# Kernel optimization log

Measured on AMD Instinct MI355X. Metric: run time of the kernel, lower is better.

The kernel has to match this reference:

```python
import jax, jax.numpy as jnp
import numpy as np

IMG = 448; P = 16; C = 3; D = 512; DC = 8; DS = 4
NH = IMG // P            # 28 patches per side
NPATCH = NH * NH         # 784
PDIM = C * P * P         # 768
BATCH = 32
EPS = 1e-5


def setup_inputs() -> dict:
    key = jax.random.key(0)
    ks = jax.random.split(key, 10)
    def lin(k, fan_in, shape):
        bound = 1.0 / np.sqrt(fan_in)
        return jax.random.uniform(k, shape, jnp.float32, -bound, bound)
    return {
        "images": jax.random.normal(ks[0], (BATCH, C, IMG, IMG), jnp.float32),
        "W_patch": lin(ks[1], PDIM, (PDIM, D)),
        "b_patch": jnp.zeros((D,), jnp.float32),
        "pos_embed": jax.random.normal(ks[2], (1, NPATCH, D), jnp.float32) * 0.02,
        "W_coord": lin(ks[3], D, (D, DC)),
        "b_coord": jnp.zeros((DC,), jnp.float32),
        "W_spinor": lin(ks[4], D, (D, DS)),
        "b_spinor": jnp.zeros((DS,), jnp.float32),
        "W_embed": lin(ks[5], DC, (DC, D)),
        "b_embed": jnp.zeros((D,), jnp.float32),
        "ln_gamma": jnp.ones((D,), jnp.float32),
        "ln_beta": jnp.zeros((D,), jnp.float32),
        "W_out": lin(ks[6], D, (D, D)),
        "b_out": jnp.zeros((D,), jnp.float32),
    }


def reference(images, W_patch, b_patch, pos_embed, W_coord, b_coord,
              W_spinor, b_spinor, W_embed, b_embed,
              ln_gamma, ln_beta, W_out, b_out):
    B = images.shape[0]
    # patchify == F.unfold(kernel=stride=P).transpose(1,2):
    # patches[b, bh*NH+bw, c*P*P + i*P + j] = images[b, c, bh*P+i, bw*P+j]
    patches = images.reshape(B, C, NH, P, NH, P)
    patches = patches.transpose(0, 2, 4, 1, 3, 5).reshape(B, NPATCH, PDIM)
    # patch embed + positional embedding  -> (B, NPATCH, D)
    x = patches @ W_patch + b_patch + pos_embed
    # manifold projection: coords (B,N,DC), spinor (B,N,DS)
    coords = x @ W_coord + b_coord
    spinor = x @ W_spinor + b_spinor
    # K0 scalar bilinear: psi^T psi -> (B, N)
    K0 = jnp.sum(spinor * spinor, axis=-1)
    # embed back from manifold coords -> (B, N, D)
    x_manifold = coords @ W_embed + b_embed
    # K0-modulated remix + residual
    x_enh = x_manifold * K0[..., None] + x
    # output projection: LayerNorm -> Linear
    mu = jnp.mean(x_enh, axis=-1, keepdims=True)
    var = jnp.mean(jnp.square(x_enh - mu), axis=-1, keepdims=True)
    x_norm = (x_enh - mu) * jax.lax.rsqrt(var + EPS) * ln_gamma + ln_beta
    return x_norm @ W_out + b_out
```

## Files before the change

kernel.cpp:

```cpp
#include <hip/hip_runtime.h>
#include <hip/hip_bf16.h>
#include <stdint.h>


typedef __bf16 bf16_t;
typedef bf16_t bf16x8 __attribute__((ext_vector_type(8)));
typedef bf16_t bf16x4 __attribute__((ext_vector_type(4)));
typedef float  f32x4  __attribute__((ext_vector_type(4)));

#define IMG     448
#define PSZ     16
#define NHP     28
#define NPATCH  784
#define PDIM    768
#define DMODEL  512
#define MROWS   25088

__device__ __forceinline__ void gload16(void* lds, const void* g) {
  __builtin_amdgcn_global_load_lds(
      (__attribute__((address_space(1))) void*)(uintptr_t)g,
      (__attribute__((address_space(3))) void*)lds,
      16, 0, 0);
}

__global__ __launch_bounds__(256) void transpose_to_bf16(
    const float* __restrict__ src, bf16_t* __restrict__ dst, int K, int N)
{
  __shared__ float t[64][65];
  const int tx = threadIdx.x;
  const int ty = threadIdx.y;
  const int bx = blockIdx.x * 64;
  const int by = blockIdx.y * 64;
  #pragma unroll
  for (int r = ty; r < 64; r += 4)
    t[r][tx] = src[(size_t)(by + r) * N + (bx + tx)];
  __syncthreads();
  #pragma unroll
  for (int r = ty; r < 64; r += 4)
    dst[(size_t)(bx + r) * K + (by + tx)] = (bf16_t)t[tx][r];
}

__global__ __launch_bounds__(256) void manifold_prep(
    const float* __restrict__ Wc, const float* __restrict__ Ws,
    bf16_t* __restrict__ Wcsg)
{
  const int idx = blockIdx.x * 256 + threadIdx.x;
  if (idx < 8192) {
    const int r = idx >> 9, n = idx & 511;
    float v = 0.f;
    if (r < 8)       v = Wc[n * 8 + r];
    else if (r < 12) v = Ws[n * 4 + (r - 8)];
    Wcsg[idx] = (bf16_t)v;
  }
}

__global__ __launch_bounds__(256) void patchify_bf16(
    const float* __restrict__ images, bf16_t* __restrict__ Apat)
{
  __shared__ bf16_t t[16][456];
  const int tid = threadIdx.x;
  const int bid = blockIdx.x;
  const int b = bid / 84, rem = bid % 84;
  const int c = rem / 28, ph = rem % 28;
  const float* src = images + ((size_t)(b * 3 + c) * IMG + ph * PSZ) * IMG;

  #pragma unroll
  for (int idx = tid; idx < 16 * 112; idx += 256) {
    const int i = idx / 112, x4 = idx % 112;
    const float4 v = *(const float4*)(src + (size_t)i * IMG + x4 * 4);
    bf16x4 w;
    w[0] = (bf16_t)v.x; w[1] = (bf16_t)v.y; w[2] = (bf16_t)v.z; w[3] = (bf16_t)v.w;
    *(bf16x4*)&t[i][x4 * 4] = w;
  }
  __syncthreads();

  const size_t mbase = (size_t)b * NPATCH + (size_t)ph * NHP;
  #pragma unroll
  for (int idx = tid; idx < 28 * 64; idx += 256) {
    const int pw = idx >> 6, e = idx & 63;
    const int i = e >> 2, j4 = e & 3;
    const bf16x4 w = *(const bf16x4*)&t[i][pw * 16 + j4 * 4];
    *(bf16x4*)&Apat[(mbase + pw) * PDIM + c * 256 + i * 16 + j4 * 4] = w;
  }
}

template<int KDIM, int EPI>
__global__ __launch_bounds__(256) void gemm_bf16(
    const bf16_t* __restrict__ A, const bf16_t* __restrict__ BT,
    const float* __restrict__ bias, const float* __restrict__ pos,
    void* __restrict__ outp)
{
  __shared__ bf16_t As[3 * 64 * 64];
  __shared__ bf16_t Bs[3 * 128 * 64];
  constexpr int ABUF = 64 * 64;
  constexpr int BBUF = 128 * 64;
  constexpr int NT = KDIM / 64;

  const int tid  = threadIdx.x;
  const int orig = blockIdx.x;
  const int wg   = (orig & 7) * 196 + (orig >> 3);
  const int n0   = (wg & 3) * 128;
  const int m0   = (wg >> 2) * 64;

  const int wave = tid >> 6, lane = tid & 63;

  const int ra = lane >> 3;
  const int ca = (lane & 7) ^ ra;
  const bf16_t* ag = A  + (size_t)(m0 + wave * 8 + ra) * KDIM + ca * 8;
  const bf16_t* bg = BT + (size_t)(n0 + wave * 8 + ra) * KDIM + ca * 8;
  const int aoff0 = (wave * 8) * 64;
  const int aoff1 = (wave * 8 + 32) * 64;
  const int boff0 = (wave * 8) * 64;
  const int boff1 = (wave * 8 + 32) * 64;
  const int boff2 = (wave * 8 + 64) * 64;
  const int boff3 = (wave * 8 + 96) * 64;

  const int wm = (wave >> 1) * 32;
  const int wn = (wave & 1) * 64;
  const int lr = lane & 15;
  const int lt = lane >> 4;

  auto STAGE = [&](int buf, int k0) {
    gload16(As + buf * ABUF + aoff0, ag + k0);
    gload16(As + buf * ABUF + aoff1, ag + 32 * KDIM + k0);
    gload16(Bs + buf * BBUF + boff0, bg + k0);
    gload16(Bs + buf * BBUF + boff1, bg + 32 * KDIM + k0);
    gload16(Bs + buf * BBUF + boff2, bg + 64 * KDIM + k0);
    gload16(Bs + buf * BBUF + boff3, bg + 96 * KDIM + k0);
  };

  STAGE(0, 0);
  STAGE(1, 64);

  f32x4 acc[2][4] = {};

  for (int t = 0; t < NT; ++t) {
    if (t < NT - 1) asm volatile("s_waitcnt vmcnt(6)" ::: "memory");
    else            asm volatile("s_waitcnt vmcnt(0)" ::: "memory");
    __builtin_amdgcn_s_barrier();
    if (t + 2 < NT) STAGE((t + 2) % 3, (t + 2) * 64);

    const bf16_t* Ab = As + (t % 3) * ABUF;
    const bf16_t* Bb = Bs + (t % 3) * BBUF;
    #pragma unroll
    for (int ks = 0; ks < 2; ++ks) {
      const int c = ks * 4 + lt;
      bf16x8 af[2], bfr[4];
      #pragma unroll
      for (int i = 0; i < 2; ++i) {
        const int row = wm + i * 16 + lr;
        af[i] = *(const bf16x8*)&Ab[row * 64 + ((c ^ (row & 7)) * 8)];
      }
      #pragma unroll
      for (int j = 0; j < 4; ++j) {
        const int row = wn + j * 16 + lr;
        bfr[j] = *(const bf16x8*)&Bb[row * 64 + ((c ^ (row & 7)) * 8)];
      }
      #pragma unroll
      for (int i = 0; i < 2; ++i)
        #pragma unroll
        for (int j = 0; j < 4; ++j)
          acc[i][j] = __builtin_amdgcn_mfma_f32_16x16x32_bf16(af[i], bfr[j], acc[i][j], 0, 0, 0);
    }
  }

  const int q4 = lt << 2;
  const int colb = n0 + wn;
  #pragma unroll
  for (int i = 0; i < 2; ++i) {
    #pragma unroll
    for (int r = 0; r < 4; ++r) {
      const int mm = m0 + wm + i * 16 + q4 + r;
      if (EPI == 0) {
        const int pp = mm % NPATCH;
        const float* pe = pos + (size_t)pp * DMODEL;
        bf16_t* orow = (bf16_t*)outp + (size_t)mm * DMODEL;
        #pragma unroll
        for (int j = 0; j < 4; ++j) {
          const int nn = colb + j * 16 + lr;
          orow[nn] = (bf16_t)(acc[i][j][r] + bias[nn] + pe[nn]);
        }
      } else {
        float* orow = (float*)outp + (size_t)mm * DMODEL;
        #pragma unroll
        for (int j = 0; j < 4; ++j) {
          const int nn = colb + j * 16 + lr;
          orow[nn] = acc[i][j][r] + bias[nn];
        }
      }
    }
  }
}

__global__ __launch_bounds__(64) void manifold_v5(
    bf16_t* __restrict__ x, const bf16_t* __restrict__ Wcsg,
    const float* __restrict__ b_coord, const float* __restrict__ b_spinor,
    const float* __restrict__ We, const float* __restrict__ be,
    const float* __restrict__ gamma, const float* __restrict__ beta)
{
  __shared__ float cbuf[16][12];

  const int lane = threadIdx.x;
  const int lr   = lane & 15;
  const int lk   = (lane >> 4) << 3;
  const int q4   = (lane >> 4) << 2;
  const int m0w  = blockIdx.x * 16;

  float bbv[4];
  #pragma unroll
  for (int r = 0; r < 4; ++r) {
    if (q4 == 0)      bbv[r] = b_coord[r];
    else if (q4 == 4) bbv[r] = b_coord[4 + r];
    else if (q4 == 8) bbv[r] = b_spinor[r];
    else              bbv[r] = 0.f;
  }

  const bf16_t* xrow = x + (size_t)(m0w + lr) * DMODEL + lk;
  const bf16_t* wrow = Wcsg + lr * DMODEL + lk;
  f32x4 acc1 = {0.f, 0.f, 0.f, 0.f};
  #pragma unroll
  for (int ks = 0; ks < 16; ++ks) {
    const bf16x8 bf = *(const bf16x8*)(xrow + ks * 32);
    const bf16x8 wf = *(const bf16x8*)(wrow + ks * 32);
    acc1 = __builtin_amdgcn_mfma_f32_16x16x32_bf16(wf, bf, acc1, 0, 0, 0);
  }
  float sv[4];
  #pragma unroll
  for (int r = 0; r < 4; ++r) sv[r] = acc1[r] + bbv[r];

  if (q4 == 8) {
    cbuf[lr][8] = sv[0] * sv[0] + sv[1] * sv[1] + sv[2] * sv[2] + sv[3] * sv[3];
  } else if (q4 == 0 || q4 == 4) {
    f32x4 st = {sv[0], sv[1], sv[2], sv[3]};
    *(f32x4*)&cbuf[lr][q4] = st;
  }
  __syncthreads();

  const int n0 = lane * 8;
  f32x4 wlo[8], whi[8];
  #pragma unroll
  for (int dc = 0; dc < 8; ++dc) {
    wlo[dc] = *(const f32x4*)&We[dc * DMODEL + n0];
    whi[dc] = *(const f32x4*)&We[dc * DMODEL + n0 + 4];
  }
  const f32x4 beL = *(const f32x4*)&be[n0];
  const f32x4 beH = *(const f32x4*)&be[n0 + 4];
  const f32x4 gL  = *(const f32x4*)&gamma[n0];
  const f32x4 gH  = *(const f32x4*)&gamma[n0 + 4];
  const f32x4 btL = *(const f32x4*)&beta[n0];
  const f32x4 btH = *(const f32x4*)&beta[n0 + 4];

  #pragma unroll 2
  for (int rr = 0; rr < 16; ++rr) {
    const size_t row = (size_t)m0w + rr;
    const bf16x8 xv = *(const bf16x8*)(x + row * DMODEL + n0);
    const f32x4 c0 = *(const f32x4*)&cbuf[rr][0];
    const f32x4 c1 = *(const f32x4*)&cbuf[rr][4];
    const float k0 = cbuf[rr][8];

    float v[8];
    float s1 = 0.f, s2 = 0.f;
    #pragma unroll
    for (int e = 0; e < 4; ++e) {
      float xm = beL[e];
      #pragma unroll
      for (int dc = 0; dc < 4; ++dc) xm += c0[dc] * wlo[dc][e];
      #pragma unroll
      for (int dc = 0; dc < 4; ++dc) xm += c1[dc] * wlo[4 + dc][e];
      const float vv = xm * k0 + (float)xv[e];
      v[e] = vv; s1 += vv; s2 += vv * vv;
    }
    #pragma unroll
    for (int e = 0; e < 4; ++e) {
      float xm = beH[e];
      #pragma unroll
      for (int dc = 0; dc < 4; ++dc) xm += c0[dc] * whi[dc][e];
      #pragma unroll
      for (int dc = 0; dc < 4; ++dc) xm += c1[dc] * whi[4 + dc][e];
      const float vv = xm * k0 + (float)xv[4 + e];
      v[4 + e] = vv; s1 += vv; s2 += vv * vv;
    }

    #pragma unroll
    for (int off = 1; off <= 32; off <<= 1) {
      s1 += __shfl_xor(s1, off, 64);
      s2 += __shfl_xor(s2, off, 64);
    }
    const float mu  = s1 * (1.f / 512.f);
    const float var = s2 * (1.f / 512.f) - mu * mu;
    const float rs  = rsqrtf(var + 1e-5f);

    bf16x8 o;
    #pragma unroll
    for (int e = 0; e < 4; ++e) {
      o[e]     = (bf16_t)((v[e]     - mu) * rs * gL[e] + btL[e]);
      o[4 + e] = (bf16_t)((v[4 + e] - mu) * rs * gH[e] + btH[e]);
    }
    *(bf16x8*)(x + row * DMODEL + n0) = o;
  }
}

extern "C" void kernel_launch(void* const* d_in, const int* in_sizes, int n_in,
                              void* d_out, int out_size, void* d_ws, size_t ws_size,
                              hipStream_t stream)
{
  const float* images    = (const float*)d_in[0];
  const float* W_patch   = (const float*)d_in[1];
  const float* b_patch   = (const float*)d_in[2];
  const float* pos_embed = (const float*)d_in[3];
  const float* W_coord   = (const float*)d_in[4];
  const float* b_coord   = (const float*)d_in[5];
  const float* W_spinor  = (const float*)d_in[6];
  const float* b_spinor  = (const float*)d_in[7];
  const float* W_embed   = (const float*)d_in[8];
  const float* b_embed   = (const float*)d_in[9];
  const float* ln_gamma  = (const float*)d_in[10];
  const float* ln_beta   = (const float*)d_in[11];
  const float* W_out     = (const float*)d_in[12];
  const float* b_out     = (const float*)d_in[13];
  float* out = (float*)d_out;

  const size_t SZ_APAT = (size_t)MROWS * PDIM * 2;
  const size_t SZ_X    = (size_t)MROWS * DMODEL * 2;
  const size_t SZ_WPT  = (size_t)DMODEL * PDIM * 2;
  const size_t SZ_WOT  = (size_t)DMODEL * DMODEL * 2;

  char* ws = (char*)d_ws;
  char* p  = ws;
  bf16_t* Apat = (bf16_t*)p;   p += SZ_APAT;
  bf16_t* x    = (bf16_t*)p;   p += SZ_X;
  bf16_t* WpT  = (bf16_t*)p;   p += SZ_WPT;
  bf16_t* WoT  = (bf16_t*)p;   p += SZ_WOT;
  bf16_t* Wcsg = (bf16_t*)p;

  hipLaunchKernelGGL(transpose_to_bf16, dim3(8, 12), dim3(64, 4), 0, stream,
                     W_patch, WpT, PDIM, DMODEL);
  hipLaunchKernelGGL(transpose_to_bf16, dim3(8, 8), dim3(64, 4), 0, stream,
                     W_out, WoT, DMODEL, DMODEL);
  hipLaunchKernelGGL(manifold_prep, dim3(32), dim3(256), 0, stream,
                     W_coord, W_spinor, Wcsg);

  hipLaunchKernelGGL(patchify_bf16, dim3(32 * 3 * 28), dim3(256), 0, stream,
                     images, Apat);
  hipLaunchKernelGGL((gemm_bf16<PDIM, 0>), dim3(1568), dim3(256), 0, stream,
                     Apat, WpT, b_patch, pos_embed, (void*)x);

  hipLaunchKernelGGL(manifold_v5, dim3(MROWS / 16), dim3(64), 0, stream,
                     x, Wcsg, b_coord, b_spinor, W_embed, b_embed, ln_gamma, ln_beta);

  hipLaunchKernelGGL((gemm_bf16<DMODEL, 1>), dim3(1568), dim3(256), 0, stream,
                     x, WoT, b_out, (const float*)nullptr, (void*)out);
}
```

Baseline: 118.5 us.

## Shrink GEMM tile to 64x64 and drop triple-buffered async pipeline

Both GEMMs move from 64x128 tiles with a three-stage global_load_lds pipeline to 64x64 tiles with a single LDS buffer, synchronised by two barriers per k-step. The grid doubles to 3136 blocks and each wave holds a 2x2 accumulator block. This cuts LDS use and registers per block, which may raise occupancy, but it gives up overlap of loads with MFMA work and reuse of the A tile across the wider N tile.

```diff
diff --git a/kernel.cpp b/kernel.cpp
--- a/kernel.cpp
+++ b/kernel.cpp
@@ -90,17 +90,15 @@
     const float* __restrict__ bias, const float* __restrict__ pos,
     void* __restrict__ outp)
 {
-  __shared__ bf16_t As[3 * 64 * 64];
-  __shared__ bf16_t Bs[3 * 128 * 64];
-  constexpr int ABUF = 64 * 64;
-  constexpr int BBUF = 128 * 64;
+  __shared__ bf16_t As[64 * 64];
+  __shared__ bf16_t Bs[64 * 64];
   constexpr int NT = KDIM / 64;
 
   const int tid  = threadIdx.x;
   const int orig = blockIdx.x;
-  const int wg   = (orig & 7) * 196 + (orig >> 3);
-  const int n0   = (wg & 3) * 128;
-  const int m0   = (wg >> 2) * 64;
+  const int wg   = (orig & 7) * 392 + (orig >> 3);
+  const int n0   = (wg & 7) * 64;
+  const int m0   = (wg >> 3) * 64;
 
   const int wave = tid >> 6, lane = tid & 63;
 
@@ -108,58 +106,45 @@
   const int ca = (lane & 7) ^ ra;
   const bf16_t* ag = A  + (size_t)(m0 + wave * 8 + ra) * KDIM + ca * 8;
   const bf16_t* bg = BT + (size_t)(n0 + wave * 8 + ra) * KDIM + ca * 8;
-  const int aoff0 = (wave * 8) * 64;
-  const int aoff1 = (wave * 8 + 32) * 64;
-  const int boff0 = (wave * 8) * 64;
-  const int boff1 = (wave * 8 + 32) * 64;
-  const int boff2 = (wave * 8 + 64) * 64;
-  const int boff3 = (wave * 8 + 96) * 64;
+  bf16_t* al0 = As + (wave * 8) * 64;
+  bf16_t* al1 = As + (wave * 8 + 32) * 64;
+  bf16_t* bl0 = Bs + (wave * 8) * 64;
+  bf16_t* bl1 = Bs + (wave * 8 + 32) * 64;
 
   const int wm = (wave >> 1) * 32;
-  const int wn = (wave & 1) * 64;
+  const int wn = (wave & 1) * 32;
   const int lr = lane & 15;
   const int lt = lane >> 4;
 
-  auto STAGE = [&](int buf, int k0) {
-    gload16(As + buf * ABUF + aoff0, ag + k0);
-    gload16(As + buf * ABUF + aoff1, ag + 32 * KDIM + k0);
-    gload16(Bs + buf * BBUF + boff0, bg + k0);
-    gload16(Bs + buf * BBUF + boff1, bg + 32 * KDIM + k0);
-    gload16(Bs + buf * BBUF + boff2, bg + 64 * KDIM + k0);
-    gload16(Bs + buf * BBUF + boff3, bg + 96 * KDIM + k0);
-  };
-
-  STAGE(0, 0);
-  STAGE(1, 64);
-
-  f32x4 acc[2][4] = {};
+  f32x4 acc[2][2] = {};
 
   for (int t = 0; t < NT; ++t) {
-    if (t < NT - 1) asm volatile("s_waitcnt vmcnt(6)" ::: "memory");
-    else            asm volatile("s_waitcnt vmcnt(0)" ::: "memory");
-    __builtin_amdgcn_s_barrier();
-    if (t + 2 < NT) STAGE((t + 2) % 3, (t + 2) * 64);
-
-    const bf16_t* Ab = As + (t % 3) * ABUF;
-    const bf16_t* Bb = Bs + (t % 3) * BBUF;
+    const int k0 = t * 64;
+    __syncthreads();
+    gload16(al0, ag + k0);
+    gload16(al1, ag + 32 * KDIM + k0);
+    gload16(bl0, bg + k0);
+    gload16(bl1, bg + 32 * KDIM + k0);
+    __syncthreads();
+
     #pragma unroll
     for (int ks = 0; ks < 2; ++ks) {
       const int c = ks * 4 + lt;
-      bf16x8 af[2], bfr[4];
+      bf16x8 af[2], bfr[2];
       #pragma unroll
       for (int i = 0; i < 2; ++i) {
         const int row = wm + i * 16 + lr;
-        af[i] = *(const bf16x8*)&Ab[row * 64 + ((c ^ (row & 7)) * 8)];
+        af[i] = *(const bf16x8*)&As[row * 64 + ((c ^ (row & 7)) * 8)];
       }
       #pragma unroll
-      for (int j = 0; j < 4; ++j) {
+      for (int j = 0; j < 2; ++j) {
         const int row = wn + j * 16 + lr;
-        bfr[j] = *(const bf16x8*)&Bb[row * 64 + ((c ^ (row & 7)) * 8)];
+        bfr[j] = *(const bf16x8*)&Bs[row * 64 + ((c ^ (row & 7)) * 8)];
       }
       #pragma unroll
       for (int i = 0; i < 2; ++i)
         #pragma unroll
-        for (int j = 0; j < 4; ++j)
+        for (int j = 0; j < 2; ++j)
           acc[i][j] = __builtin_amdgcn_mfma_f32_16x16x32_bf16(af[i], bfr[j], acc[i][j], 0, 0, 0);
     }
   }
@@ -176,14 +161,14 @@
         const float* pe = pos + (size_t)pp * DMODEL;
         bf16_t* orow = (bf16_t*)outp + (size_t)mm * DMODEL;
         #pragma unroll
-        for (int j = 0; j < 4; ++j) {
+        for (int j = 0; j < 2; ++j) {
           const int nn = colb + j * 16 + lr;
           orow[nn] = (bf16_t)(acc[i][j][r] + bias[nn] + pe[nn]);
         }
       } else {
         float* orow = (float*)outp + (size_t)mm * DMODEL;
         #pragma unroll
-        for (int j = 0; j < 4; ++j) {
+        for (int j = 0; j < 2; ++j) {
           const int nn = colb + j * 16 + lr;
           orow[nn] = acc[i][j][r] + bias[nn];
         }
@@ -342,12 +327,12 @@
 
   hipLaunchKernelGGL(patchify_bf16, dim3(32 * 3 * 28), dim3(256), 0, stream,
                      images, Apat);
-  hipLaunchKernelGGL((gemm_bf16<PDIM, 0>), dim3(1568), dim3(256), 0, stream,
+  hipLaunchKernelGGL((gemm_bf16<PDIM, 0>), dim3(3136), dim3(256), 0, stream,
                      Apat, WpT, b_patch, pos_embed, (void*)x);
 
   hipLaunchKernelGGL(manifold_v5, dim3(MROWS / 16), dim3(64), 0, stream,
                      x, Wcsg, b_coord, b_spinor, W_embed, b_embed, ln_gamma, ln_beta);
 
-  hipLaunchKernelGGL((gemm_bf16<DMODEL, 1>), dim3(1568), dim3(256), 0, stream,
+  hipLaunchKernelGGL((gemm_bf16<DMODEL, 1>), dim3(3136), dim3(256), 0, stream,
                      x, WoT, b_out, (const float*)nullptr, (void*)out);
 }
```

Result: faster. 114.2 us (-3.6%).
